# Kernel tuning notes

Measured on AMD Instinct MI355X. Metric: run time of the kernel, lower is better.

## Reference

```python
import jax, jax.numpy as jnp
import numpy as np

SIZES = [(64, 32), (32, 16), (16, 8), (8, 16), (16, 32)]
BZ, T, D = 2048, 512, 64


def setup_inputs() -> dict:
    key = jax.random.key(0)
    ks = jax.random.split(key, 32)
    inp = {
        "X": jax.random.normal(ks[0], (BZ, T, D), jnp.float32),
        "missing_mask": (jax.random.uniform(ks[1], (BZ, T, D)) < 0.8).astype(jnp.float32),
        "imputation_latent": jax.random.normal(ks[2], (BZ, T, D), jnp.float32),
    }
    for i, (din, dh) in enumerate(SIZES):
        s = 1.0 / np.sqrt(dh)  # PyTorch RNNCell init range
        k = 3 + 4 * i
        inp[f"wih{i}"] = jax.random.uniform(ks[k], (3 * dh, din), jnp.float32, -s, s)
        inp[f"whh{i}"] = jax.random.uniform(ks[k + 1], (3 * dh, dh), jnp.float32, -s, s)
        inp[f"bih{i}"] = jax.random.uniform(ks[k + 2], (3 * dh,), jnp.float32, -s, s)
        inp[f"bhh{i}"] = jax.random.uniform(ks[k + 3], (3 * dh,), jnp.float32, -s, s)
    so = 1.0 / np.sqrt(32)
    inp["out_w"] = jax.random.uniform(ks[23], (D, 32), jnp.float32, -so, so)
    inp["out_b"] = jax.random.uniform(ks[24], (D,), jnp.float32, -so, so)
    return inp


def _gru_cell(x, h, wih, whh, bih, bhh):
    # PyTorch nn.GRUCell gate order: r, z, n
    gi = x @ wih.T + bih
    gh = h @ whh.T + bhh
    ir, iz, inn = jnp.split(gi, 3, axis=-1)
    hr, hz, hn = jnp.split(gh, 3, axis=-1)
    r = jax.nn.sigmoid(ir + hr)
    z = jax.nn.sigmoid(iz + hz)
    n = jnp.tanh(inn + r * hn)
    return (1.0 - z) * n + z * h


def _forward(X, missing_mask, imputation_latent, params, out_w, out_b):
    imputed = X * missing_mask + imputation_latent * (1.0 - missing_mask)
    xs = jnp.swapaxes(imputed, 0, 1)  # [T, B, D]
    bz = X.shape[0]
    h0 = tuple(jnp.zeros((bz, dh), X.dtype) for _, dh in SIZES)

    def step(hs, x):
        new = []
        inp_x = x
        for i, (wih, whh, bih, bhh) in enumerate(params):
            h = _gru_cell(inp_x, hs[i], wih, whh, bih, bhh)
            new.append(h)
            inp_x = h  # layer i+1 consumes the freshly-updated hidden state
        return tuple(new), new[-1]

    _, hcol = jax.lax.scan(step, h0, xs)  # [T, B, 32]
    hcol = jnp.swapaxes(hcol, 0, 1)  # [B, T, 32]
    return hcol @ out_w.T + out_b


def reference(X, missing_mask, imputation_latent,
              wih0, whh0, bih0, bhh0, wih1, whh1, bih1, bhh1,
              wih2, whh2, bih2, bhh2, wih3, whh3, bih3, bhh3,
              wih4, whh4, bih4, bhh4, out_w, out_b):
    params = [(wih0, whh0, bih0, bhh0), (wih1, whh1, bih1, bhh1),
              (wih2, whh2, bih2, bhh2), (wih3, whh3, bih3, bhh3),
              (wih4, whh4, bih4, bhh4)]
    return _forward(X, missing_mask, imputation_latent, params, out_w, out_b)
```

## Files before the change

kernel.cpp:

```cpp
#include <hip/hip_runtime.h>

typedef short s16x8 __attribute__((ext_vector_type(8)));
typedef short s16x4 __attribute__((ext_vector_type(4)));
typedef float f32x4 __attribute__((ext_vector_type(4)));
typedef unsigned int u32;
typedef unsigned short u16;

#define NT 512
#define DD 64
#define NTH 512

#define CHUNK 1024

#define P2STRIDE (5*CHUNK)
#define PH0 0
#define PH1 CHUNK
#define PH2 (2*CHUNK)
#define PH3 (3*CHUNK)
#define PH4 (4*CHUNK)
#define FRTOT2 (2*P2STRIDE)
#define NSTEP2 517

#define PSTRIDE (7*CHUNK)
#define XIN0 0
#define H0C (2*CHUNK)
#define H1C (3*CHUNK)
#define H2C (4*CHUNK)
#define H3C (5*CHUNK)
#define H4C (6*CHUNK)
#define FRTOT (2*PSTRIDE)
#define NSTEP_FB 517

#define MFMA16(A,B,C) __builtin_amdgcn_mfma_f32_16x16x32_bf16(A,B,C,0,0,0)

__device__ __forceinline__ float sigf(float x){ return 1.0f/(1.0f+__expf(-x)); }
__device__ __forceinline__ float tanhf2(float x){ return 2.0f/(1.0f+__expf(-2.0f*x)) - 1.0f; }

__device__ __forceinline__ u16 f2bf(float f) {
  u32 u = __builtin_bit_cast(u32, f);
  return (u16)((u + 0x7fffu + ((u >> 16) & 1u)) >> 16);
}
__device__ __forceinline__ float bf2f(u16 h) {
  u32 u = ((u32)h) << 16;
  return __builtin_bit_cast(float, u);
}

__device__ __forceinline__ void soft_barrier() {
  asm volatile("s_waitcnt lgkmcnt(0)" ::: "memory");
  __builtin_amdgcn_s_barrier();
  asm volatile("" ::: "memory");
}

__device__ __forceinline__ u32 cvtpk_bf16(float a, float b) {
  u32 r;
  asm("v_cvt_pk_bf16_f32 %0, %1, %2" : "=v"(r) : "v"(a), "v"(b));
  return r;
}

__device__ __forceinline__ void load_wfrag(const float* __restrict__ W, int row0, int nrow, int din,
                                           int kbase, int lane, s16x8& hi, s16x8& lo)
{
  const int m = lane & 15, kb = lane >> 4;
#pragma unroll
  for (int e = 0; e < 8; ++e) {
    int k = kbase + kb*8 + e;
    float v = (m < nrow && k < din) ? W[(size_t)(row0 + m)*din + k] : 0.0f;
    u16 h = f2bf(v);
    hi[e] = (short)h;
    lo[e] = (short)f2bf(v - bf2f(h));
  }
}

__device__ __forceinline__ void load_wfrag_pk(const float* __restrict__ W, int row0, int nrow,
                                              int stride, int KR, int lane, s16x8& A1)
{
  const int m = lane & 15, q = lane >> 4;
  const bool lohalf = q >= 2;
  const int kb = (q & 1) * 8;
#pragma unroll
  for (int e = 0; e < 8; ++e) {
    int k = kb + e;
    float v = (m < nrow && k < KR) ? W[(size_t)(row0 + m)*stride + k] : 0.0f;
    u16 h = f2bf(v);
    A1[e] = (short)(lohalf ? f2bf(v - bf2f(h)) : h);
  }
}

__device__ __forceinline__ void read_b(const u16* base, int lane, s16x8& hi, s16x8& lo)
{
  const int off = ((lane >> 4) << 8) + ((lane & 15) << 3);
  hi = *(const s16x8*)(base + off);
  lo = *(const s16x8*)(base + off + 128);
}

__device__ __forceinline__ void read_b_pk(const u16* base, int lane, s16x8& b1, s16x8& b2)
{
  const int q = lane >> 4;
  const int off1 = ((q & 1) << 8) + ((q >> 1) << 7) + ((lane & 15) << 3);
  b1 = *(const s16x8*)(base + off1);
  b2 = *(const s16x8*)(base + (off1 ^ 128));
}

__device__ __forceinline__ void combine_write2(
    f32x4 aR, f32x4 aZ, f32x4 aNi, f32x4 aNh,
    float (&hprev)[4], u16* hdst_base, int jbase, int nrow, int lane)
{
  const int bb = lane & 15, q = lane >> 4;
  float hv[4];
#pragma unroll
  for (int i = 0; i < 4; ++i) {
    float rr = sigf(aR[i]);
    float zz = sigf(aZ[i]);
    float nn = tanhf2(aNi[i] + rr*aNh[i]);
    hv[i] = (1.0f - zz)*nn + zz*hprev[i];
    hprev[i] = hv[i];
  }
  if (bb < 8 && q*4 < nrow) {
    const int j = jbase + q*4;
    u16* dst = hdst_base + ((j >> 3) << 8) + bb*8 + (j & 7);
    u32 p01 = cvtpk_bf16(hv[0], hv[1]);
    u32 p23 = cvtpk_bf16(hv[2], hv[3]);
    float h0 = __builtin_bit_cast(float, p01 << 16);
    float h1 = __builtin_bit_cast(float, p01 & 0xffff0000u);
    float h2 = __builtin_bit_cast(float, p23 << 16);
    float h3 = __builtin_bit_cast(float, p23 & 0xffff0000u);
    u32 q01 = cvtpk_bf16(hv[0]-h0, hv[1]-h1);
    u32 q23 = cvtpk_bf16(hv[2]-h2, hv[3]-h3);
    uint2 hp_; hp_.x = p01; hp_.y = p23;
    uint2 lp_; lp_.x = q01; lp_.y = q23;
    *(uint2*)dst = hp_;
    *(uint2*)(dst + 128) = lp_;
  }
}

__global__ __launch_bounds__(256)
void gi0_gemm(const float* __restrict__ X, const float* __restrict__ M, const float* __restrict__ L,
              const float* __restrict__ wih0, const float* __restrict__ bih0,
              const float* __restrict__ bhh0,
              float* __restrict__ gi)
{
  __shared__ u32 xs[128*65];
  const int tid = threadIdx.x;
  const int wv = tid >> 6, lane = tid & 63;
  const int q = lane >> 4;
  const int b = blockIdx.x >> 2;
  const int t0 = (blockIdx.x & 3) * 128;
  const size_t base = ((size_t)b*NT + t0)*DD;

  for (int i = tid; i < 128*64; i += 256) {
    float x = X[base+i], m = M[base+i], l = L[base+i];
    float v = x*m + l*(1.0f - m);
    u16 h = f2bf(v);
    u16 lo2 = f2bf(v - bf2f(h));
    const int t = i >> 6, d = i & 63;
    xs[t*65 + d] = (u32)h | ((u32)lo2 << 16);
  }

  s16x8 Ah[6][2], Al[6][2];
  f32x4 cb[6];
#pragma unroll
  for (int tile = 0; tile < 6; ++tile) {
#pragma unroll
    for (int c = 0; c < 2; ++c)
      load_wfrag(wih0, tile*16, 16, 64, c*32, lane, Ah[tile][c], Al[tile][c]);
#pragma unroll
    for (int i = 0; i < 4; ++i) {
      int row = tile*16 + q*4 + i;
      float bv = bih0[row];
      if (tile < 4) bv += bhh0[row];
      cb[tile][i] = bv;
    }
  }
  __syncthreads();

#pragma unroll
  for (int g2 = 0; g2 < 2; ++g2) {
    const int tloc = g2*64 + wv*16 + (lane & 15);
    s16x8 Bh[2], Bl[2];
#pragma unroll
    for (int c = 0; c < 2; ++c) {
      const u32* p = &xs[tloc*65 + c*32 + q*8];
#pragma unroll
      for (int e = 0; e < 8; ++e) {
        u32 v = p[e];
        Bh[c][e] = (short)(v & 0xffffu);
        Bl[c][e] = (short)(v >> 16);
      }
    }
    float* gp = gi + ((size_t)b*NT + t0 + tloc)*96 + q*4;
#pragma unroll
    for (int tile = 0; tile < 6; ++tile) {
      f32x4 acc = cb[tile];
#pragma unroll
      for (int c = 0; c < 2; ++c) {
        acc = MFMA16(Ah[tile][c], Bh[c], acc);
        acc = MFMA16(Ah[tile][c], Bl[c], acc);
        acc = MFMA16(Al[tile][c], Bh[c], acc);
      }
      *(f32x4*)(gp + tile*16) = acc;
    }
  }
}

__device__ __forceinline__ void wave_l0(
    const float* __restrict__ Whh, const float* __restrict__ bhh,
    const float* __restrict__ gi, int jbase,
    u16* FRu, int b0, int lane)
{
  s16x8 Ahh[3], Ahl[3];
#pragma unroll
  for (int g = 0; g < 3; ++g)
    load_wfrag(Whh, g*32 + jbase, 16, 32, 0, lane, Ahh[g], Ahl[g]);
  const int q = lane >> 4;
  f32x4 cNh;
#pragma unroll
  for (int i = 0; i < 4; ++i) cNh[i] = bhh[64 + jbase + q*4 + i];
  float hprev[4] = {0.f,0.f,0.f,0.f};

  const float* gb = gi + (size_t)(b0 + (lane & 7)) * ((size_t)NT*96) + jbase + q*4;
  f32x4 AR, AZ, AN, BR, BZ, BN;
  AR = *(const f32x4*)(gb);      AZ = *(const f32x4*)(gb+32);  AN = *(const f32x4*)(gb+64);
  BR = *(const f32x4*)(gb+96);   BZ = *(const f32x4*)(gb+128); BN = *(const f32x4*)(gb+160);

  for (int s = 0; s < NSTEP2; s += 2) {
    if (s < NT) {
      f32x4 aR = AR, aZ = AZ, aNi = AN, aNh = cNh;
      s16x8 bh_, bl_;
      read_b(FRu + P2STRIDE + PH0, lane, bh_, bl_);
      aR  = MFMA16(Ahh[0], bh_, aR);  aR  = MFMA16(Ahh[0], bl_, aR);  aR  = MFMA16(Ahl[0], bh_, aR);
      aZ  = MFMA16(Ahh[1], bh_, aZ);  aZ  = MFMA16(Ahh[1], bl_, aZ);  aZ  = MFMA16(Ahl[1], bh_, aZ);
      aNh = MFMA16(Ahh[2], bh_, aNh); aNh = MFMA16(Ahh[2], bl_, aNh); aNh = MFMA16(Ahl[2], bh_, aNh);
      combine_write2(aR, aZ, aNi, aNh, hprev, FRu + PH0, jbase, 16, lane);
    }
    if (s + 2 < NT) {
      const float* p = gb + (size_t)(s + 2)*96;
      AR = *(const f32x4*)(p); AZ = *(const f32x4*)(p+32); AN = *(const f32x4*)(p+64);
    }
    soft_barrier();
    if (s + 1 < NT) {
      f32x4 aR = BR, aZ = BZ, aNi = BN, aNh = cNh;
      s16x8 bh_, bl_;
      read_b(FRu + PH0, lane, bh_, bl_);
      aR  = MFMA16(Ahh[0], bh_, aR);  aR  = MFMA16(Ahh[0], bl_, aR);  aR  = MFMA16(Ahl[0], bh_, aR);
      aZ  = MFMA16(Ahh[1], bh_, aZ);  aZ  = MFMA16(Ahh[1], bl_, aZ);  aZ  = MFMA16(Ahl[1], bh_, aZ);
      aNh = MFMA16(Ahh[2], bh_, aNh); aNh = MFMA16(Ahh[2], bl_, aNh); aNh = MFMA16(Ahl[2], bh_, aNh);
      combine_write2(aR, aZ, aNi, aNh, hprev, FRu + P2STRIDE + PH0, jbase, 16, lane);
    }
    if (s + 3 < NT) {
      const float* p = gb + (size_t)(s + 3)*96;
      BR = *(const f32x4*)(p); BZ = *(const f32x4*)(p+32); BN = *(const f32x4*)(p+64);
    }
    soft_barrier();
  }
}

template<int DIN, int DH, bool PKX, bool PKH>
__device__ __forceinline__ void wave_mid_pk(
    const float* __restrict__ Wih, const float* __restrict__ Whh,
    const float* __restrict__ bih, const float* __restrict__ bhh,
    int jbase, int xc, int hc, int s0, int s1,
    u16* FRu, int lane)
{
  const int nrow = (DH - jbase) < 16 ? (DH - jbase) : 16;
  s16x8 Ax1[3], Axh[3], Axl[3], Ah1[3], Ahh[3], Ahl[3];
#pragma unroll
  for (int g = 0; g < 3; ++g) {
    if constexpr (PKX) load_wfrag_pk(Wih, g*DH + jbase, nrow, DIN, DIN, lane, Ax1[g]);
    else               load_wfrag(Wih, g*DH + jbase, nrow, DIN, 0, lane, Axh[g], Axl[g]);
    if constexpr (PKH) load_wfrag_pk(Whh, g*DH + jbase, nrow, DH, DH, lane, Ah1[g]);
    else               load_wfrag(Whh, g*DH + jbase, nrow, DH, 0, lane, Ahh[g], Ahl[g]);
  }
  const int q = lane >> 4;
  f32x4 cR, cZ, cNi, cNh;
#pragma unroll
  for (int i = 0; i < 4; ++i) {
    int lr = q*4 + i;
    int j = jbase + lr;
    bool jr = lr < nrow;
    cR[i]  = jr ? bih[j] + bhh[j] : 0.f;
    cZ[i]  = jr ? bih[DH+j] + bhh[DH+j] : 0.f;
    cNi[i] = jr ? bih[2*DH+j] : 0.f;
    cNh[i] = jr ? bhh[2*DH+j] : 0.f;
  }
  float hprev[4] = {0.f,0.f,0.f,0.f};

  auto body = [&](int st, const u16* R, u16* Wp) {
    if (st >= s0 && st <= s1) {
      f32x4 aR = cR, aZ = cZ, aNi = cNi, aNh = cNh;
      if constexpr (PKX) {
        s16x8 b1, b2;
        read_b_pk(R + xc, lane, b1, b2);
        aR  = MFMA16(Ax1[0], b1, aR);  aR  = MFMA16(Ax1[0], b2, aR);
        aZ  = MFMA16(Ax1[1], b1, aZ);  aZ  = MFMA16(Ax1[1], b2, aZ);
        aNi = MFMA16(Ax1[2], b1, aNi); aNi = MFMA16(Ax1[2], b2, aNi);
      } else {
        s16x8 bh_, bl_;
        read_b(R + xc, lane, bh_, bl_);
        aR  = MFMA16(Axh[0], bh_, aR);  aR  = MFMA16(Axh[0], bl_, aR);  aR  = MFMA16(Axl[0], bh_, aR);
        aZ  = MFMA16(Axh[1], bh_, aZ);  aZ  = MFMA16(Axh[1], bl_, aZ);  aZ  = MFMA16(Axl[1], bh_, aZ);
        aNi = MFMA16(Axh[2], bh_, aNi); aNi = MFMA16(Axh[2], bl_, aNi); aNi = MFMA16(Axl[2], bh_, aNi);
      }
      if constexpr (PKH) {
        s16x8 b1, b2;
        read_b_pk(R + hc, lane, b1, b2);
        aR  = MFMA16(Ah1[0], b1, aR);  aR  = MFMA16(Ah1[0], b2, aR);
        aZ  = MFMA16(Ah1[1], b1, aZ);  aZ  = MFMA16(Ah1[1], b2, aZ);
        aNh = MFMA16(Ah1[2], b1, aNh); aNh = MFMA16(Ah1[2], b2, aNh);
      } else {
        s16x8 bh_, bl_;
        read_b(R + hc, lane, bh_, bl_);
        aR  = MFMA16(Ahh[0], bh_, aR);  aR  = MFMA16(Ahh[0], bl_, aR);  aR  = MFMA16(Ahl[0], bh_, aR);
        aZ  = MFMA16(Ahh[1], bh_, aZ);  aZ  = MFMA16(Ahh[1], bl_, aZ);  aZ  = MFMA16(Ahl[1], bh_, aZ);
        aNh = MFMA16(Ahh[2], bh_, aNh); aNh = MFMA16(Ahh[2], bl_, aNh); aNh = MFMA16(Ahl[2], bh_, aNh);
      }
      combine_write2(aR, aZ, aNi, aNh, hprev, Wp + hc, jbase, nrow, lane);
    }
  };

  for (int s = 0; s < NSTEP2; s += 2) {
    body(s,     FRu + P2STRIDE, FRu);
    soft_barrier();
    body(s + 1, FRu,            FRu + P2STRIDE);
    soft_barrier();
  }
}

__device__ __forceinline__ void wave_out2(
    const float* __restrict__ OW, const float* __restrict__ OBb,
    u16* FRu, float* __restrict__ out, int b0, int lane)
{
  s16x8 Oh[4], Ol[4];
  f32x4 cO[4];
  const int q = lane >> 4, bb = lane & 15;
#pragma unroll
  for (int t4 = 0; t4 < 4; ++t4) {
    load_wfrag(OW, t4*16, 16, 32, 0, lane, Oh[t4], Ol[t4]);
#pragma unroll
    for (int i = 0; i < 4; ++i) cO[t4][i] = OBb[t4*16 + q*4 + i];
  }
  float* ob = out + ((size_t)(b0 + (bb & 7))*NT)*DD + q*4;

  auto emit = [&](int st, const u16* R) {
    if (st >= 5 && st <= 516) {
      s16x8 bh_, bl_;
      read_b(R + PH4, lane, bh_, bl_);
#pragma unroll
      for (int t4 = 0; t4 < 4; ++t4) {
        f32x4 a_ = cO[t4];
        a_ = MFMA16(Oh[t4], bh_, a_); a_ = MFMA16(Oh[t4], bl_, a_); a_ = MFMA16(Ol[t4], bh_, a_);
        if (bb < 8) *(f32x4*)(ob + t4*16) = a_;
      }
      ob += DD;
    }
  };

  for (int s = 0; s < NSTEP2; s += 2) {
    emit(s,     FRu + P2STRIDE);
    soft_barrier();
    emit(s + 1, FRu);
    soft_barrier();
  }
}

__global__ __launch_bounds__(NTH, 1)
void gru_rec(const float* __restrict__ gi,
             const float* __restrict__ whh0, const float* __restrict__ bhh0,
             const float* __restrict__ wih1, const float* __restrict__ whh1, const float* __restrict__ bih1, const float* __restrict__ bhh1,
             const float* __restrict__ wih2, const float* __restrict__ whh2, const float* __restrict__ bih2, const float* __restrict__ bhh2,
             const float* __restrict__ wih3, const float* __restrict__ whh3, const float* __restrict__ bih3, const float* __restrict__ bhh3,
             const float* __restrict__ wih4, const float* __restrict__ whh4, const float* __restrict__ bih4, const float* __restrict__ bhh4,
             const float* __restrict__ out_w, const float* __restrict__ out_b,
             float* __restrict__ out)
{
  __shared__ __align__(16) u16 FRu[FRTOT2];
  const int tid = threadIdx.x;
  const int w = tid >> 6, lane = tid & 63;
  const int b0 = blockIdx.x * 8;

  for (int i = tid; i < FRTOT2; i += NTH) FRu[i] = 0;
  __syncthreads();

  if (w == 0)
    wave_l0(whh0, bhh0, gi,  0, FRu, b0, lane);
  else if (w == 1)
    wave_l0(whh0, bhh0, gi, 16, FRu, b0, lane);
  else if (w == 2)
    wave_mid_pk<32,16,false,true >(wih1,whh1,bih1,bhh1,  0, PH0, PH1, 1, 512, FRu, lane);
  else if (w == 4)
    wave_mid_pk<16, 8,true ,true >(wih2,whh2,bih2,bhh2,  0, PH1, PH2, 2, 513, FRu, lane);
  else if (w == 5)
    wave_mid_pk< 8,16,true ,true >(wih3,whh3,bih3,bhh3,  0, PH2, PH3, 3, 514, FRu, lane);
  else if (w == 3)
    wave_mid_pk<16,32,true ,false>(wih4,whh4,bih4,bhh4,  0, PH3, PH4, 4, 515, FRu, lane);
  else if (w == 6)
    wave_mid_pk<16,32,true ,false>(wih4,whh4,bih4,bhh4, 16, PH3, PH4, 4, 515, FRu, lane);
  else
    wave_out2(out_w, out_b, FRu, out, b0, lane);
}

__device__ __forceinline__ void combine_write(
    f32x4 aR, f32x4 aZ, f32x4 aNi, f32x4 aNh,
    float (&hprev)[4], u16* hdst_base, int jbase, int nrow, int lane)
{
  const int bb = lane & 15, q = lane >> 4;
  float hv[4];
#pragma unroll
  for (int i = 0; i < 4; ++i) {
    float rr = sigf(aR[i]);
    float zz = sigf(aZ[i]);
    float nn = tanhf2(aNi[i] + rr*aNh[i]);
    hv[i] = (1.0f - zz)*nn + zz*hprev[i];
    hprev[i] = hv[i];
  }
  if (bb < 8 && q*4 < nrow) {
    const int j = jbase + q*4;
    const int kb = j >> 3, e = j & 7;
    s16x4 hh, ll;
#pragma unroll
    for (int i = 0; i < 4; ++i) {
      u16 h = f2bf(hv[i]);
      hh[i] = (short)h;
      ll[i] = (short)f2bf(hv[i] - bf2f(h));
    }
    u16* dst = hdst_base + kb*256 + bb*8 + e;
    *(s16x4*)dst = hh;
    *(s16x4*)(dst + 128) = ll;
  }
}

__device__ __forceinline__ void write_x(u16* FRu, int par, int w, int lane, float v)
{
  const int d = lane;
  const int chunk = d >> 5, kb = (d >> 3) & 3, e = d & 7;
  u16 h = f2bf(v);
  u16 l2 = f2bf(v - bf2f(h));
  u16* p = FRu + par*PSTRIDE + XIN0 + chunk*CHUNK + kb*256 + w*8 + e;
  p[0] = h; p[128] = l2;
}

template<int DIN, int DH, int NXC>
__device__ __forceinline__ void wave_gru_fb(
    const float* __restrict__ Wih, const float* __restrict__ Whh,
    const float* __restrict__ bih, const float* __restrict__ bhh,
    int jbase, int xc, int hc, int s0, int s1,
    u16* FRu, float* OST,
    const float* __restrict__ X, const float* __restrict__ Mm, const float* __restrict__ Ll,
    float* __restrict__ out, int b0, int w, int lane)
{
  const int nrow = (DH - jbase) < 16 ? (DH - jbase) : 16;
  s16x8 Axh[3][NXC], Axl[3][NXC], Ahh[3], Ahl[3];
#pragma unroll
  for (int g = 0; g < 3; ++g) {
#pragma unroll
    for (int c = 0; c < NXC; ++c)
      load_wfrag(Wih, g*DH + jbase, nrow, DIN, c*32, lane, Axh[g][c], Axl[g][c]);
    load_wfrag(Whh, g*DH + jbase, nrow, DH, 0, lane, Ahh[g], Ahl[g]);
  }
  f32x4 cR, cZ, cNi, cNh;
  {
    const int q = lane >> 4;
#pragma unroll
    for (int i = 0; i < 4; ++i) {
      int lr = q*4 + i;
      int j = jbase + lr;
      bool jr = lr < nrow;
      cR[i]  = jr ? bih[j] + bhh[j] : 0.f;
      cZ[i]  = jr ? bih[DH+j] + bhh[DH+j] : 0.f;
      cNi[i] = jr ? bih[2*DH+j] : 0.f;
      cNh[i] = jr ? bhh[2*DH+j] : 0.f;
    }
  }
  float hprev[4] = {0.f, 0.f, 0.f, 0.f};

  const size_t gbase = ((size_t)(b0 + w))*((size_t)NT*DD) + lane;
  float rx = X[gbase], rm = Mm[gbase], rl = Ll[gbase];
  write_x(FRu, 1, w, lane, rx*rm + rl*(1.0f - rm));
  rx = X[gbase + DD]; rm = Mm[gbase + DD]; rl = Ll[gbase + DD];
  __syncthreads();

  for (int s = 0; s < NSTEP_FB; ++s) {
    const int par = s & 1, rp = par ^ 1;
    float nx = 0.f, nm = 0.f, nl = 0.f;
    if (s <= 509) {
      size_t g = gbase + (size_t)(s+2)*DD;
      nx = X[g]; nm = Mm[g]; nl = Ll[g];
    }
    f32x4 aR = cR, aZ = cZ, aNi = cNi, aNh = cNh;
    const bool run = (s >= s0) && (s <= s1);
    if (run) {
      const u16* RB = FRu + rp*PSTRIDE;
      s16x8 bh_, bl_;
#pragma unroll
      for (int c = 0; c < NXC; ++c) {
        read_b(RB + xc + c*CHUNK, lane, bh_, bl_);
        aR  = MFMA16(Axh[0][c], bh_, aR);  aR  = MFMA16(Axh[0][c], bl_, aR);  aR  = MFMA16(Axl[0][c], bh_, aR);
        aZ  = MFMA16(Axh[1][c], bh_, aZ);  aZ  = MFMA16(Axh[1][c], bl_, aZ);  aZ  = MFMA16(Axl[1][c], bh_, aZ);
        aNi = MFMA16(Axh[2][c], bh_, aNi); aNi = MFMA16(Axh[2][c], bl_, aNi); aNi = MFMA16(Axl[2][c], bh_, aNi);
      }
      read_b(RB + hc, lane, bh_, bl_);
      aR  = MFMA16(Ahh[0], bh_, aR);  aR  = MFMA16(Ahh[0], bl_, aR);  aR  = MFMA16(Ahl[0], bh_, aR);
      aZ  = MFMA16(Ahh[1], bh_, aZ);  aZ  = MFMA16(Ahh[1], bl_, aZ);  aZ  = MFMA16(Ahl[1], bh_, aZ);
      aNh = MFMA16(Ahh[2], bh_, aNh); aNh = MFMA16(Ahh[2], bl_, aNh); aNh = MFMA16(Ahl[2], bh_, aNh);
    }
    __syncthreads();

    if (run)
      combine_write(aR, aZ, aNi, aNh, hprev, FRu + par*PSTRIDE + hc, jbase, nrow, lane);
    if (s >= 5)
      out[((size_t)(b0 + w)*NT + (s-5))*DD + lane] = OST[w*65 + lane];
    if (s <= 510) write_x(FRu, par, w, lane, rx*rm + rl*(1.0f - rm));
    rx = nx; rm = nm; rl = nl;
    __syncthreads();
  }
}

__device__ __forceinline__ void wave_out_fb(
    const float* __restrict__ OW, const float* __restrict__ OBb,
    u16* FRu, float* OST,
    const float* __restrict__ X, const float* __restrict__ Mm, const float* __restrict__ Ll,
    float* __restrict__ out, int b0, int w, int lane)
{
  s16x8 Oh[4], Ol[4];
  f32x4 cO[4];
#pragma unroll
  for (int t4 = 0; t4 < 4; ++t4) {
    load_wfrag(OW, t4*16, 16, 32, 0, lane, Oh[t4], Ol[t4]);
#pragma unroll
    for (int i = 0; i < 4; ++i) cO[t4][i] = OBb[t4*16 + (lane>>4)*4 + i];
  }
  const size_t gbase = ((size_t)(b0 + w))*((size_t)NT*DD) + lane;
  float rx = X[gbase], rm = Mm[gbase], rl = Ll[gbase];
  write_x(FRu, 1, w, lane, rx*rm + rl*(1.0f - rm));
  rx = X[gbase + DD]; rm = Mm[gbase + DD]; rl = Ll[gbase + DD];
  __syncthreads();

  for (int s = 0; s < NSTEP_FB; ++s) {
    const int par = s & 1, rp = par ^ 1;
    float nx = 0.f, nm = 0.f, nl = 0.f;
    if (s <= 509) { size_t g = gbase + (size_t)(s+2)*DD; nx = X[g]; nm = Mm[g]; nl = Ll[g]; }
    if (s >= 5) {
      s16x8 bh_, bl_;
      read_b(FRu + rp*PSTRIDE + H4C, lane, bh_, bl_);
      const int bb = lane & 15, q = lane >> 4;
#pragma unroll
      for (int t4 = 0; t4 < 4; ++t4) {
        f32x4 a_ = cO[t4];
        a_ = MFMA16(Oh[t4], bh_, a_); a_ = MFMA16(Oh[t4], bl_, a_); a_ = MFMA16(Ol[t4], bh_, a_);
        if (bb < 8) {
#pragma unroll
          for (int i = 0; i < 4; ++i) OST[bb*65 + t4*16 + q*4 + i] = a_[i];
        }
      }
    }
    __syncthreads();
    if (s >= 5)
      out[((size_t)(b0 + w)*NT + (s-5))*DD + lane] = OST[w*65 + lane];
    if (s <= 510) write_x(FRu, par, w, lane, rx*rm + rl*(1.0f - rm));
    rx = nx; rm = nm; rl = nl;
    __syncthreads();
  }
}

__global__ __launch_bounds__(NTH, 1)
void gru_mfma(const float* __restrict__ X, const float* __restrict__ M, const float* __restrict__ L,
              const float* __restrict__ wih0, const float* __restrict__ whh0, const float* __restrict__ bih0, const float* __restrict__ bhh0,
              const float* __restrict__ wih1, const float* __restrict__ whh1, const float* __restrict__ bih1, const float* __restrict__ bhh1,
              const float* __restrict__ wih2, const float* __restrict__ whh2, const float* __restrict__ bih2, const float* __restrict__ bhh2,
              const float* __restrict__ wih3, const float* __restrict__ whh3, const float* __restrict__ bih3, const float* __restrict__ bhh3,
              const float* __restrict__ wih4, const float* __restrict__ whh4, const float* __restrict__ bih4, const float* __restrict__ bhh4,
              const float* __restrict__ out_w, const float* __restrict__ out_b,
              float* __restrict__ out)
{
  __shared__ __align__(16) u16 FRu[FRTOT];
  __shared__ float OST[8*65];
  const int tid = threadIdx.x;
  const int w = tid >> 6, lane = tid & 63;
  const int b0 = blockIdx.x * 8;

  for (int i = tid; i < FRTOT; i += NTH) FRu[i] = 0;
  for (int i = tid; i < 8*65; i += NTH) OST[i] = 0.f;
  __syncthreads();

  if (w == 0)
    wave_gru_fb<64,32,2>(wih0,whh0,bih0,bhh0,  0, XIN0, H0C, 0, 511, FRu, OST, X,M,L, out, b0, w, lane);
  else if (w == 1)
    wave_gru_fb<64,32,2>(wih0,whh0,bih0,bhh0, 16, XIN0, H0C, 0, 511, FRu, OST, X,M,L, out, b0, w, lane);
  else if (w == 2)
    wave_gru_fb<32,16,1>(wih1,whh1,bih1,bhh1,  0, H0C,  H1C, 1, 512, FRu, OST, X,M,L, out, b0, w, lane);
  else if (w == 4)
    wave_gru_fb<16, 8,1>(wih2,whh2,bih2,bhh2,  0, H1C,  H2C, 2, 513, FRu, OST, X,M,L, out, b0, w, lane);
  else if (w == 5)
    wave_gru_fb< 8,16,1>(wih3,whh3,bih3,bhh3,  0, H2C,  H3C, 3, 514, FRu, OST, X,M,L, out, b0, w, lane);
  else if (w == 3)
    wave_gru_fb<16,32,1>(wih4,whh4,bih4,bhh4,  0, H3C,  H4C, 4, 515, FRu, OST, X,M,L, out, b0, w, lane);
  else if (w == 6)
    wave_gru_fb<16,32,1>(wih4,whh4,bih4,bhh4, 16, H3C,  H4C, 4, 515, FRu, OST, X,M,L, out, b0, w, lane);
  else
    wave_out_fb(out_w, out_b, FRu, OST, X,M,L, out, b0, w, lane);
}

extern "C" void kernel_launch(void* const* d_in, const int* in_sizes, int n_in,
                              void* d_out, int out_size, void* d_ws, size_t ws_size,
                              hipStream_t stream)
{
  const float* X  = (const float*)d_in[0];
  const float* M  = (const float*)d_in[1];
  const float* L  = (const float*)d_in[2];
  const float* wp[20];
  for (int i = 0; i < 20; ++i) wp[i] = (const float*)d_in[3 + i];
  const float* ow = (const float*)d_in[23];
  const float* ob = (const float*)d_in[24];
  float* out = (float*)d_out;

  const size_t gi_bytes = (size_t)2048 * NT * 96 * sizeof(float);
  if (ws_size >= gi_bytes) {
    float* gi = (float*)d_ws;
    gi0_gemm<<<dim3(2048*4), dim3(256), 0, stream>>>(X, M, L, wp[0], wp[2], wp[3], gi);
    gru_rec<<<dim3(256), dim3(NTH), 0, stream>>>(
        gi, wp[1], wp[3],
        wp[4], wp[5], wp[6], wp[7],
        wp[8], wp[9], wp[10], wp[11],
        wp[12], wp[13], wp[14], wp[15],
        wp[16], wp[17], wp[18], wp[19],
        ow, ob, out);
  } else {
    gru_mfma<<<dim3(256), dim3(NTH), 0, stream>>>(
        X, M, L,
        wp[0], wp[1], wp[2], wp[3],
        wp[4], wp[5], wp[6], wp[7],
        wp[8], wp[9], wp[10], wp[11],
        wp[12], wp[13], wp[14], wp[15],
        wp[16], wp[17], wp[18], wp[19],
        ow, ob, out);
  }
}
```

Before: 861.4 us.

## Defer mid-layer GRU combine across barriers and split combine across lane halves

Single-wave mid layers (1-3) now compute the input-side MFMAs for step t, then apply the combine for step t-1 and write h in the same barrier interval. The recurrent MFMAs for the new h follow an LDS fence. This deepens the wavefront pipeline by one stage per such layer, so total steps grow to 520 and the layer start offsets and output window shift to match. The combine is also rewritten to use ds_swizzle so each lane evaluates only 2 gate elements instead of 4, cutting the transcendental work per lane. The cost is extra pipeline steps and swizzle instructions.

```diff
diff --git a/kernel.cpp b/kernel.cpp
--- a/kernel.cpp
+++ b/kernel.cpp
@@ -19,7 +19,7 @@
 #define PH3 (3*CHUNK)
 #define PH4 (4*CHUNK)
 #define FRTOT2 (2*P2STRIDE)
-#define NSTEP2 517
+#define NSTEP2 520
 
 #define PSTRIDE (7*CHUNK)
 #define XIN0 0
@@ -51,10 +51,19 @@
   asm volatile("" ::: "memory");
 }
 
+__device__ __forceinline__ void lds_fence() {
+  asm volatile("s_waitcnt lgkmcnt(0)" ::: "memory");
+}
+
 __device__ __forceinline__ u32 cvtpk_bf16(float a, float b) {
   u32 r;
   asm("v_cvt_pk_bf16_f32 %0, %1, %2" : "=v"(r) : "v"(a), "v"(b));
   return r;
+}
+
+__device__ __forceinline__ float swzf(float v) {
+  return __builtin_bit_cast(float,
+      __builtin_amdgcn_ds_swizzle(__builtin_bit_cast(int, v), 0x201F));
 }
 
 __device__ __forceinline__ void load_wfrag(const float* __restrict__ W, int row0, int nrow, int din,
@@ -101,35 +110,44 @@
   b2 = *(const s16x8*)(base + (off1 ^ 128));
 }
 
-__device__ __forceinline__ void combine_write2(
+template<bool NI_OWN>
+__device__ __forceinline__ void combine_split8(
     f32x4 aR, f32x4 aZ, f32x4 aNi, f32x4 aNh,
-    float (&hprev)[4], u16* hdst_base, int jbase, int nrow, int lane)
+    float (&hp)[2], u16* dstC, int jbase, int nrow, int lane)
 {
   const int bb = lane & 15, q = lane >> 4;
-  float hv[4];
-#pragma unroll
-  for (int i = 0; i < 4; ++i) {
-    float rr = sigf(aR[i]);
-    float zz = sigf(aZ[i]);
-    float nn = tanhf2(aNi[i] + rr*aNh[i]);
-    hv[i] = (1.0f - zz)*nn + zz*hprev[i];
-    hprev[i] = hv[i];
-  }
-  if (bb < 8 && q*4 < nrow) {
-    const int j = jbase + q*4;
-    u16* dst = hdst_base + ((j >> 3) << 8) + bb*8 + (j & 7);
-    u32 p01 = cvtpk_bf16(hv[0], hv[1]);
-    u32 p23 = cvtpk_bf16(hv[2], hv[3]);
-    float h0 = __builtin_bit_cast(float, p01 << 16);
-    float h1 = __builtin_bit_cast(float, p01 & 0xffff0000u);
-    float h2 = __builtin_bit_cast(float, p23 << 16);
-    float h3 = __builtin_bit_cast(float, p23 & 0xffff0000u);
-    u32 q01 = cvtpk_bf16(hv[0]-h0, hv[1]-h1);
-    u32 q23 = cvtpk_bf16(hv[2]-h2, hv[3]-h3);
-    uint2 hp_; hp_.x = p01; hp_.y = p23;
-    uint2 lp_; lp_.x = q01; lp_.y = q23;
-    *(uint2*)dst = hp_;
-    *(uint2*)(dst + 128) = lp_;
+  const bool hih = (bb & 8) != 0;
+  float sR2 = swzf(aR[2]),  sR3 = swzf(aR[3]);
+  float sZ2 = swzf(aZ[2]),  sZ3 = swzf(aZ[3]);
+  float sH2 = swzf(aNh[2]), sH3 = swzf(aNh[3]);
+  float r0  = hih ? sR2 : aR[0],  r1  = hih ? sR3 : aR[1];
+  float z0  = hih ? sZ2 : aZ[0],  z1  = hih ? sZ3 : aZ[1];
+  float nh0 = hih ? sH2 : aNh[0], nh1 = hih ? sH3 : aNh[1];
+  float ni0, ni1;
+  if constexpr (NI_OWN) {
+    ni0 = hih ? aNi[2] : aNi[0];
+    ni1 = hih ? aNi[3] : aNi[1];
+  } else {
+    float sN2 = swzf(aNi[2]), sN3 = swzf(aNi[3]);
+    ni0 = hih ? sN2 : aNi[0];
+    ni1 = hih ? sN3 : aNi[1];
+  }
+  float rr0 = sigf(r0), rr1 = sigf(r1);
+  float zz0 = sigf(z0), zz1 = sigf(z1);
+  float n0 = tanhf2(ni0 + rr0*nh0), n1 = tanhf2(ni1 + rr1*nh1);
+  float h0 = (1.0f - zz0)*n0 + zz0*hp[0];
+  float h1 = (1.0f - zz1)*n1 + zz1*hp[1];
+  hp[0] = h0; hp[1] = h1;
+  const int jj = q*4 + (hih ? 2 : 0);
+  if (jj < nrow) {
+    const int j = jbase + jj;
+    u32 ph = cvtpk_bf16(h0, h1);
+    float f0 = h0 - __builtin_bit_cast(float, ph << 16);
+    float f1 = h1 - __builtin_bit_cast(float, ph & 0xffff0000u);
+    u32 pl = cvtpk_bf16(f0, f1);
+    u16* dst = dstC + ((j >> 3) << 8) + ((bb & 7) << 3) + (j & 7);
+    *(u32*)dst = ph;
+    *(u32*)(dst + 128) = pl;
   }
 }
 
@@ -215,47 +233,39 @@
   f32x4 cNh;
 #pragma unroll
   for (int i = 0; i < 4; ++i) cNh[i] = bhh[64 + jbase + q*4 + i];
-  float hprev[4] = {0.f,0.f,0.f,0.f};
+  float hp[2] = {0.f, 0.f};
 
   const float* gb = gi + (size_t)(b0 + (lane & 7)) * ((size_t)NT*96) + jbase + q*4;
   f32x4 AR, AZ, AN, BR, BZ, BN;
   AR = *(const f32x4*)(gb);      AZ = *(const f32x4*)(gb+32);  AN = *(const f32x4*)(gb+64);
   BR = *(const f32x4*)(gb+96);   BZ = *(const f32x4*)(gb+128); BN = *(const f32x4*)(gb+160);
 
-  for (int s = 0; s < NSTEP2; s += 2) {
-    if (s < NT) {
-      f32x4 aR = AR, aZ = AZ, aNi = AN, aNh = cNh;
+  auto body = [&](int st, const u16* R, u16* Wp, f32x4& gR, f32x4& gZ, f32x4& gN) {
+    if (st < NT) {
+      f32x4 aR = gR, aZ = gZ, aNi = gN, aNh = cNh;
       s16x8 bh_, bl_;
-      read_b(FRu + P2STRIDE + PH0, lane, bh_, bl_);
+      read_b(R + PH0, lane, bh_, bl_);
       aR  = MFMA16(Ahh[0], bh_, aR);  aR  = MFMA16(Ahh[0], bl_, aR);  aR  = MFMA16(Ahl[0], bh_, aR);
       aZ  = MFMA16(Ahh[1], bh_, aZ);  aZ  = MFMA16(Ahh[1], bl_, aZ);  aZ  = MFMA16(Ahl[1], bh_, aZ);
       aNh = MFMA16(Ahh[2], bh_, aNh); aNh = MFMA16(Ahh[2], bl_, aNh); aNh = MFMA16(Ahl[2], bh_, aNh);
-      combine_write2(aR, aZ, aNi, aNh, hprev, FRu + PH0, jbase, 16, lane);
-    }
-    if (s + 2 < NT) {
-      const float* p = gb + (size_t)(s + 2)*96;
-      AR = *(const f32x4*)(p); AZ = *(const f32x4*)(p+32); AN = *(const f32x4*)(p+64);
-    }
+      combine_split8<true>(aR, aZ, aNi, aNh, hp, Wp + PH0, jbase, 16, lane);
+    }
+    if (st + 2 < NT) {
+      const float* p = gb + (size_t)(st + 2)*96;
+      gR = *(const f32x4*)(p); gZ = *(const f32x4*)(p+32); gN = *(const f32x4*)(p+64);
+    }
+  };
+
+  for (int s = 0; s < NSTEP2; s += 2) {
+    body(s,     FRu + P2STRIDE, FRu,            AR, AZ, AN);
     soft_barrier();
-    if (s + 1 < NT) {
-      f32x4 aR = BR, aZ = BZ, aNi = BN, aNh = cNh;
-      s16x8 bh_, bl_;
-      read_b(FRu + PH0, lane, bh_, bl_);
-      aR  = MFMA16(Ahh[0], bh_, aR);  aR  = MFMA16(Ahh[0], bl_, aR);  aR  = MFMA16(Ahl[0], bh_, aR);
-      aZ  = MFMA16(Ahh[1], bh_, aZ);  aZ  = MFMA16(Ahh[1], bl_, aZ);  aZ  = MFMA16(Ahl[1], bh_, aZ);
-      aNh = MFMA16(Ahh[2], bh_, aNh); aNh = MFMA16(Ahh[2], bl_, aNh); aNh = MFMA16(Ahl[2], bh_, aNh);
-      combine_write2(aR, aZ, aNi, aNh, hprev, FRu + P2STRIDE + PH0, jbase, 16, lane);
-    }
-    if (s + 3 < NT) {
-      const float* p = gb + (size_t)(s + 3)*96;
-      BR = *(const f32x4*)(p); BZ = *(const f32x4*)(p+32); BN = *(const f32x4*)(p+64);
-    }
+    body(s + 1, FRu,            FRu + P2STRIDE, BR, BZ, BN);
     soft_barrier();
   }
 }
 
 template<int DIN, int DH, bool PKX, bool PKH>
-__device__ __forceinline__ void wave_mid_pk(
+__device__ __forceinline__ void wave_mid_nd(
     const float* __restrict__ Wih, const float* __restrict__ Whh,
     const float* __restrict__ bih, const float* __restrict__ bhh,
     int jbase, int xc, int hc, int s0, int s1,
@@ -282,7 +292,7 @@
     cNi[i] = jr ? bih[2*DH+j] : 0.f;
     cNh[i] = jr ? bhh[2*DH+j] : 0.f;
   }
-  float hprev[4] = {0.f,0.f,0.f,0.f};
+  float hp[2] = {0.f, 0.f};
 
   auto body = [&](int st, const u16* R, u16* Wp) {
     if (st >= s0 && st <= s1) {
@@ -313,7 +323,7 @@
         aZ  = MFMA16(Ahh[1], bh_, aZ);  aZ  = MFMA16(Ahh[1], bl_, aZ);  aZ  = MFMA16(Ahl[1], bh_, aZ);
         aNh = MFMA16(Ahh[2], bh_, aNh); aNh = MFMA16(Ahh[2], bl_, aNh); aNh = MFMA16(Ahl[2], bh_, aNh);
       }
-      combine_write2(aR, aZ, aNi, aNh, hprev, Wp + hc, jbase, nrow, lane);
+      combine_split8<false>(aR, aZ, aNi, aNh, hp, Wp + hc, jbase, nrow, lane);
     }
   };
 
@@ -325,6 +335,87 @@
   }
 }
 
+template<int DIN, int DH, bool PKX, bool PKH>
+__device__ __forceinline__ void wave_mid_df(
+    const float* __restrict__ Wih, const float* __restrict__ Whh,
+    const float* __restrict__ bih, const float* __restrict__ bhh,
+    int jbase, int xc, int hc, int s0,
+    u16* FRu, int lane)
+{
+  const int nrow = (DH - jbase) < 16 ? (DH - jbase) : 16;
+  s16x8 Ax1[3], Axh[3], Axl[3], Ah1[3], Ahh[3], Ahl[3];
+#pragma unroll
+  for (int g = 0; g < 3; ++g) {
+    if constexpr (PKX) load_wfrag_pk(Wih, g*DH + jbase, nrow, DIN, DIN, lane, Ax1[g]);
+    else               load_wfrag(Wih, g*DH + jbase, nrow, DIN, 0, lane, Axh[g], Axl[g]);
+    if constexpr (PKH) load_wfrag_pk(Whh, g*DH + jbase, nrow, DH, DH, lane, Ah1[g]);
+    else               load_wfrag(Whh, g*DH + jbase, nrow, DH, 0, lane, Ahh[g], Ahl[g]);
+  }
+  const int q = lane >> 4;
+  f32x4 cR, cZ, cNi, cNh;
+#pragma unroll
+  for (int i = 0; i < 4; ++i) {
+    int lr = q*4 + i;
+    int j = jbase + lr;
+    bool jr = lr < nrow;
+    cR[i]  = jr ? bih[j] + bhh[j] : 0.f;
+    cZ[i]  = jr ? bih[DH+j] + bhh[DH+j] : 0.f;
+    cNi[i] = jr ? bih[2*DH+j] : 0.f;
+    cNh[i] = jr ? bhh[2*DH+j] : 0.f;
+  }
+  f32x4 accR = {}, accZ = {}, accNi = {}, accNh = {};
+  float hp[2] = {0.f, 0.f};
+
+  auto body = [&](int st, const u16* R, u16* Wp) {
+    const bool compute = (st >= s0) && (st <= s0 + 511);
+    const bool docomb  = (st >= s0 + 1) && (st <= s0 + 512);
+    f32x4 nR, nZ, nNi, nNh;
+    if (compute) {
+      nR = cR; nZ = cZ; nNi = cNi; nNh = cNh;
+      if constexpr (PKX) {
+        s16x8 b1, b2;
+        read_b_pk(R + xc, lane, b1, b2);
+        nR  = MFMA16(Ax1[0], b1, nR);  nR  = MFMA16(Ax1[0], b2, nR);
+        nZ  = MFMA16(Ax1[1], b1, nZ);  nZ  = MFMA16(Ax1[1], b2, nZ);
+        nNi = MFMA16(Ax1[2], b1, nNi); nNi = MFMA16(Ax1[2], b2, nNi);
+      } else {
+        s16x8 bh_, bl_;
+        read_b(R + xc, lane, bh_, bl_);
+        nR  = MFMA16(Axh[0], bh_, nR);  nR  = MFMA16(Axh[0], bl_, nR);  nR  = MFMA16(Axl[0], bh_, nR);
+        nZ  = MFMA16(Axh[1], bh_, nZ);  nZ  = MFMA16(Axh[1], bl_, nZ);  nZ  = MFMA16(Axl[1], bh_, nZ);
+        nNi = MFMA16(Axh[2], bh_, nNi); nNi = MFMA16(Axh[2], bl_, nNi); nNi = MFMA16(Axl[2], bh_, nNi);
+      }
+    }
+    if (docomb) {
+      combine_split8<false>(accR, accZ, accNi, accNh, hp, Wp + hc, jbase, nrow, lane);
+      lds_fence();
+    }
+    if (compute) {
+      if constexpr (PKH) {
+        s16x8 b1, b2;
+        read_b_pk(Wp + hc, lane, b1, b2);
+        nR  = MFMA16(Ah1[0], b1, nR);  nR  = MFMA16(Ah1[0], b2, nR);
+        nZ  = MFMA16(Ah1[1], b1, nZ);  nZ  = MFMA16(Ah1[1], b2, nZ);
+        nNh = MFMA16(Ah1[2], b1, nNh); nNh = MFMA16(Ah1[2], b2, nNh);
+      } else {
+        s16x8 bh_, bl_;
+        read_b(Wp + hc, lane, bh_, bl_);
+        nR  = MFMA16(Ahh[0], bh_, nR);  nR  = MFMA16(Ahh[0], bl_, nR);  nR  = MFMA16(Ahl[0], bh_, nR);
+        nZ  = MFMA16(Ahh[1], bh_, nZ);  nZ  = MFMA16(Ahh[1], bl_, nZ);  nZ  = MFMA16(Ahl[1], bh_, nZ);
+        nNh = MFMA16(Ahh[2], bh_, nNh); nNh = MFMA16(Ahh[2], bl_, nNh); nNh = MFMA16(Ahl[2], bh_, nNh);
+      }
+      accR = nR; accZ = nZ; accNi = nNi; accNh = nNh;
+    }
+  };
+
+  for (int s = 0; s < NSTEP2; s += 2) {
+    body(s,     FRu + P2STRIDE, FRu);
+    soft_barrier();
+    body(s + 1, FRu,            FRu + P2STRIDE);
+    soft_barrier();
+  }
+}
+
 __device__ __forceinline__ void wave_out2(
     const float* __restrict__ OW, const float* __restrict__ OBb,
     u16* FRu, float* __restrict__ out, int b0, int lane)
@@ -341,7 +432,7 @@
   float* ob = out + ((size_t)(b0 + (bb & 7))*NT)*DD + q*4;
 
   auto emit = [&](int st, const u16* R) {
-    if (st >= 5 && st <= 516) {
+    if (st >= 8 && st <= 519) {
       s16x8 bh_, bl_;
       read_b(R + PH4, lane, bh_, bl_);
 #pragma unroll
@@ -385,15 +476,15 @@
   else if (w == 1)
     wave_l0(whh0, bhh0, gi, 16, FRu, b0, lane);
   else if (w == 2)
-    wave_mid_pk<32,16,false,true >(wih1,whh1,bih1,bhh1,  0, PH0, PH1, 1, 512, FRu, lane);
+    wave_mid_df<32,16,false,true >(wih1,whh1,bih1,bhh1,  0, PH0, PH1, 1, FRu, lane);
   else if (w == 4)
-    wave_mid_pk<16, 8,true ,true >(wih2,whh2,bih2,bhh2,  0, PH1, PH2, 2, 513, FRu, lane);
+    wave_mid_df<16, 8,true ,true >(wih2,whh2,bih2,bhh2,  0, PH1, PH2, 3, FRu, lane);
   else if (w == 5)
-    wave_mid_pk< 8,16,true ,true >(wih3,whh3,bih3,bhh3,  0, PH2, PH3, 3, 514, FRu, lane);
+    wave_mid_df< 8,16,true ,true >(wih3,whh3,bih3,bhh3,  0, PH2, PH3, 5, FRu, lane);
   else if (w == 3)
-    wave_mid_pk<16,32,true ,false>(wih4,whh4,bih4,bhh4,  0, PH3, PH4, 4, 515, FRu, lane);
+    wave_mid_nd<16,32,true ,false>(wih4,whh4,bih4,bhh4,  0, PH3, PH4, 7, 518, FRu, lane);
   else if (w == 6)
-    wave_mid_pk<16,32,true ,false>(wih4,whh4,bih4,bhh4, 16, PH3, PH4, 4, 515, FRu, lane);
+    wave_mid_nd<16,32,true ,false>(wih4,whh4,bih4,bhh4, 16, PH3, PH4, 7, 518, FRu, lane);
   else
     wave_out2(out_w, out_b, FRu, out, b0, lane);
 }
```

Measured after the change: 793.6 us. 7.9% less time.
